# Optimization experiments

Hardware: AMD Instinct MI355X
Metric: run time of the kernel (lower is better)

Reference implementation:

```python
import jax, jax.numpy as jnp
import numpy as np

B, H, L, D = 2, 16, 2048, 64


def setup_inputs() -> dict:
    key = jax.random.key(0)
    kq, kk, kv = jax.random.split(key, 3)
    queries = jax.random.normal(kq, (B, H, L, D), dtype=jnp.float32)
    keys = jax.random.normal(kk, (B, H, L, D), dtype=jnp.float32)
    values = jax.random.normal(kv, (B, H, L, D), dtype=jnp.float32)
    # causal mask: True = masked (as consumed by masked_fill in the original)
    attn_mask = jnp.triu(jnp.ones((L, L), dtype=bool), k=1)
    return {"queries": queries, "keys": keys, "values": values, "attn_mask": attn_mask}


def reference(queries, keys, values, attn_mask):
    D_ = queries.shape[-1]
    scale = 1.0 / jnp.sqrt(jnp.asarray(D_, dtype=queries.dtype))
    # [B,H,Lq,Lk] score matrix (faithfully materialized as in the original)
    scores = jnp.einsum("bhqd,bhkd->bhqk", queries, keys) * scale
    scores = jnp.where(attn_mask, jnp.asarray(-1e9, dtype=scores.dtype), scores)
    attention = jax.nn.softmax(scores, axis=-1)
    # dropout rate = 0.0 (inference); identity
    out = jnp.einsum("bhqk,bhkd->bhqd", attention, values)
    return out
```

## Files before the change

kernel.cpp:

```cpp
#include <hip/hip_runtime.h>


constexpr int Lq = 2048;
constexpr int Dh = 64;
constexpr int QB = 64;
constexpr int KV = 64;
constexpr int RSTR = 144;
constexpr int IMG  = 64 * RSTR;
constexpr int TILEB = 2 * IMG;

typedef __attribute__((ext_vector_type(16))) float f32x16;
typedef __attribute__((ext_vector_type(4))) float f32x4;
typedef __attribute__((ext_vector_type(8))) unsigned short u16x8;
typedef __attribute__((ext_vector_type(4))) unsigned int u32x4;
typedef __attribute__((ext_vector_type(8))) __bf16 bf16x8;

__device__ __forceinline__ unsigned short f2bf(float f) {
  __bf16 h = (__bf16)f;
  return __builtin_bit_cast(unsigned short, h);
}
__device__ __forceinline__ unsigned pack2(float a, float b) {
  return (unsigned)f2bf(a) | ((unsigned)f2bf(b) << 16);
}
__device__ __forceinline__ f32x16 mfma32(u16x8 a, u16x8 b, f32x16 c) {
  return __builtin_amdgcn_mfma_f32_32x32x16_bf16(
      __builtin_bit_cast(bf16x8, a), __builtin_bit_cast(bf16x8, b), c, 0, 0, 0);
}
__device__ __forceinline__ void plswap(unsigned a, unsigned b,
                                       unsigned& wlo, unsigned& whi) {
#if __has_builtin(__builtin_amdgcn_permlane32_swap)
  auto r = __builtin_amdgcn_permlane32_swap((int)a, (int)b, false, false);
  wlo = (unsigned)r[0];
  whi = (unsigned)r[1];
#else
  const int hh = (threadIdx.x >> 5) & 1;
  unsigned pa = (unsigned)__shfl_xor((int)a, 32);
  unsigned pb = (unsigned)__shfl_xor((int)b, 32);
  wlo = hh ? pb : a;
  whi = hh ? b : pa;
#endif
}
__device__ __forceinline__ void glds16(const void* g, void* l) {
  __builtin_amdgcn_global_load_lds(
      (const __attribute__((address_space(1))) unsigned int*)g,
      (__attribute__((address_space(3))) unsigned int*)l, 16, 0, 0);
}

__global__ __launch_bounds__(256, 2)
void repack(const float* __restrict__ K, const float* __restrict__ V,
            unsigned char* __restrict__ W) {
  __shared__ unsigned short Vl[64][72];

  const int tid = threadIdx.x;
  const int bt  = blockIdx.x;
  const int bh  = bt >> 5;
  const int tl  = bt & 31;
  const size_t src = (size_t)bh * Lq * Dh + (size_t)tl * KV * Dh;
  unsigned char* img = W + (size_t)bt * TILEB;

  {
    const int kv = tid >> 2;
    const int c  = (tid & 3) * 2;
    const float* kp = K + src + (size_t)kv * Dh + c * 8;
    f32x4 a = *(const f32x4*)kp;
    f32x4 b = *(const f32x4*)(kp + 4);
    f32x4 cc = *(const f32x4*)(kp + 8);
    f32x4 d = *(const f32x4*)(kp + 12);
    u16x8 lo, hi;
    #pragma unroll
    for (int j = 0; j < 4; ++j) {
      lo[j] = f2bf(a[j]); lo[4 + j] = f2bf(b[j]);
      hi[j] = f2bf(cc[j]); hi[4 + j] = f2bf(d[j]);
    }
    *(u16x8*)(img + kv * RSTR + c * 16)      = lo;
    *(u16x8*)(img + kv * RSTR + c * 16 + 16) = hi;
  }
  {
    const int kv = tid >> 2;
    const int d0 = (tid & 3) * 16;
    const float* vp = V + src + (size_t)kv * Dh + d0;
    f32x4 a = *(const f32x4*)vp;
    f32x4 b = *(const f32x4*)(vp + 4);
    f32x4 cc = *(const f32x4*)(vp + 8);
    f32x4 d = *(const f32x4*)(vp + 12);
    u16x8 lo, hi;
    #pragma unroll
    for (int j = 0; j < 4; ++j) {
      lo[j] = f2bf(a[j]); lo[4 + j] = f2bf(b[j]);
      hi[j] = f2bf(cc[j]); hi[4 + j] = f2bf(d[j]);
    }
    *(u16x8*)&Vl[kv][d0]     = lo;
    *(u16x8*)&Vl[kv][d0 + 8] = hi;
  }
  __syncthreads();
  {
    const int d = tid >> 2;
    const int c = (tid & 3) * 2;
    u16x8 lo, hi;
    #pragma unroll
    for (int e = 0; e < 8; ++e) { lo[e] = Vl[c * 8 + e][d]; hi[e] = Vl[c * 8 + 8 + e][d]; }
    *(u16x8*)(img + IMG + d * RSTR + c * 16)       = lo;
    *(u16x8*)(img + IMG + d * RSTR + (c + 1) * 16) = hi;
  }
}

__global__ __launch_bounds__(256, 4)
void fattn_fwd(const float* __restrict__ Q, const unsigned char* __restrict__ W,
               float* __restrict__ O) {
  __shared__ __align__(16) unsigned char sm[2][TILEB];

  const int tid  = threadIdx.x;
  const int lane = tid & 63;
  const int w    = tid >> 6;
  const int l31  = lane & 31;
  const int h    = lane >> 5;
  const int qg   = w >> 1;
  const int kh   = w & 1;

  const int bid = blockIdx.x;
  const int xcd = bid & 7;
  const int s_  = bid >> 3;
  const int u   = s_ & 31;
  const int k   = s_ >> 5;
  const int bh  = xcd * 4 + k;
  const int qt  = (k & 1) ? u : (31 - u);
  const int qb  = qt * QB;
  const int n   = qt + 1;
  const size_t base = (size_t)bh * Lq * Dh;

  u16x8 qc[4];
  {
    const float* qp = Q + base + (size_t)(qb + qg * 32 + l31) * Dh + h * 8;
    #pragma unroll
    for (int dc = 0; dc < 4; ++dc) {
      f32x4 lo = *(const f32x4*)(qp + dc * 16);
      f32x4 hi = *(const f32x4*)(qp + dc * 16 + 4);
      u16x8 f;
      #pragma unroll
      for (int j = 0; j < 4; ++j) { f[j] = f2bf(lo[j]); f[4 + j] = f2bf(hi[j]); }
      qc[dc] = f;
    }
  }

  auto issue = [&](int t, int c) {
    const unsigned char* g = W + (size_t)(bh * 32 + t) * TILEB;
    unsigned char* dst = &sm[c][0];
    #pragma unroll
    for (int r = 0; r < 4; ++r)
      glds16(g + r * 4096 + w * 1024 + (lane << 4),
             dst + r * 4096 + w * 1024);
    if (w < 2)
      glds16(g + 16384 + w * 1024 + (lane << 4),
             dst + 16384 + w * 1024);
  };

  f32x16 accO0, accO1;
  #pragma unroll
  for (int i = 0; i < 16; ++i) { accO0[i] = 0.f; accO1[i] = 0.f; }
  float ls0 = 0.f, ls1 = 0.f, ls2 = 0.f, ls3 = 0.f;

  const float C1 = 0.125f * 1.4426950408889634f;
  const float C0 = -10.0f * 1.4426950408889634f;

  issue(0, 0);
  __syncthreads();

  for (int t = 0; t < n; ++t) {
    const int cur = t & 1;
    if (t + 1 < n) issue(t + 1, cur ^ 1);

    const unsigned char* smK = &sm[cur][0];
    const unsigned char* smV = &sm[cur][0] + IMG;
    const int kv0  = t * KV + kh * 32;
    const int qmin = qb + qg * 32;

    if (kv0 <= qmin + 31) {
      f32x16 s;
      #pragma unroll
      for (int i = 0; i < 16; ++i) s[i] = 0.f;
      __builtin_amdgcn_s_setprio(1);
      #pragma unroll
      for (int dc = 0; dc < 4; ++dc) {
        u16x8 kf = *(const u16x8*)(smK + (kh * 32 + l31) * RSTR + (dc * 2 + h) * 16);
        s = mfma32(kf, qc[dc], s);
      }
      __builtin_amdgcn_s_setprio(0);

      float p[16];
      if ((kv0 + 31) > qmin) {
        const int qrow = qmin + l31;
        #pragma unroll
        for (int r = 0; r < 16; ++r) {
          float e = __builtin_amdgcn_exp2f(s[r] * C1 + C0);
          const int kvg = kv0 + (r & 3) + 8 * (r >> 2) + 4 * h;
          p[r] = (kvg <= qrow) ? e : 0.0f;
        }
      } else {
        #pragma unroll
        for (int r = 0; r < 16; ++r)
          p[r] = __builtin_amdgcn_exp2f(s[r] * C1 + C0);
      }
      ls0 += (p[0] + p[1]) + (p[2] + p[3]);
      ls1 += (p[4] + p[5]) + (p[6] + p[7]);
      ls2 += (p[8] + p[9]) + (p[10] + p[11]);
      ls3 += (p[12] + p[13]) + (p[14] + p[15]);

      unsigned pk[4][2];
      #pragma unroll
      for (int q4 = 0; q4 < 4; ++q4) {
        pk[q4][0] = pack2(p[q4 * 4 + 0], p[q4 * 4 + 1]);
        pk[q4][1] = pack2(p[q4 * 4 + 2], p[q4 * 4 + 3]);
      }
      __builtin_amdgcn_s_setprio(1);
      #pragma unroll
      for (int c2 = 0; c2 < 2; ++c2) {
        unsigned w0, w1, w2, w3;
        plswap(pk[2 * c2][0], pk[2 * c2 + 1][0], w0, w2);
        plswap(pk[2 * c2][1], pk[2 * c2 + 1][1], w1, w3);
        u32x4 pw = {w0, w1, w2, w3};
        u16x8 pf = __builtin_bit_cast(u16x8, pw);
        const int vchunk = (kh * 4 + c2 * 2 + h) * 16;
        u16x8 vf0 = *(const u16x8*)(smV + l31 * RSTR + vchunk);
        u16x8 vf1 = *(const u16x8*)(smV + (32 + l31) * RSTR + vchunk);
        accO0 = mfma32(vf0, pf, accO0);
        accO1 = mfma32(vf1, pf, accO1);
      }
      __builtin_amdgcn_s_setprio(0);
    }
    __syncthreads();
  }

  const float lsum = (ls0 + ls1) + (ls2 + ls3);
  float* Mrg = (float*)&sm[0][0];
  if (kh == 1) {
    float* m = Mrg + (qg * 64 + lane) * 33;
    #pragma unroll
    for (int r = 0; r < 16; ++r) { m[r] = accO0[r]; m[16 + r] = accO1[r]; }
    m[32] = lsum;
  }
  __syncthreads();
  if (kh == 0) {
    const float* m = Mrg + (qg * 64 + lane) * 33;
    float ls = lsum + m[32];
    ls += __shfl_xor(ls, 32);
    const float inv = 1.0f / ls;
    float* op = O + base + (size_t)(qb + qg * 32 + l31) * Dh;
    #pragma unroll
    for (int r = 0; r < 16; ++r) {
      const int d = (r & 3) + 8 * (r >> 2) + 4 * h;
      op[d]      = (accO0[r] + m[r]) * inv;
      op[32 + d] = (accO1[r] + m[16 + r]) * inv;
    }
  }
}

extern "C" void kernel_launch(void* const* d_in, const int* in_sizes, int n_in,
                              void* d_out, int out_size, void* d_ws, size_t ws_size,
                              hipStream_t stream) {
  const float* Q = (const float*)d_in[0];
  const float* K = (const float*)d_in[1];
  const float* V = (const float*)d_in[2];
  float* O = (float*)d_out;
  unsigned char* W = (unsigned char*)d_ws;

  repack<<<dim3(1024), dim3(256), 0, stream>>>(K, V, W);
  fattn_fwd<<<dim3(1024), dim3(256), 0, stream>>>(Q, W, O);
}
```

Measured before the change: 50.82 us.

## Load K/V fragments directly from global into registers, dropping LDS staging

The repack step now writes K and V tiles in a fragment-major layout, so each lane's MFMA operand is one contiguous 16-byte chunk. The attention kernel then reads K and V fragments straight from global memory into registers with a software double buffer, instead of staging whole tiles in LDS with global_load_lds. Each wave also runs only its own causal tile count, which removes the per-tile block barriers. The cost is redundant global/L2 reads across waves, since the two q-group waves share K/V, and higher register pressure, so launch bounds drop to 3 blocks per CU.

```diff
diff --git a/kernel.cpp b/kernel.cpp
--- a/kernel.cpp
+++ b/kernel.cpp
@@ -5,9 +5,8 @@
 constexpr int Dh = 64;
 constexpr int QB = 64;
 constexpr int KV = 64;
-constexpr int RSTR = 144;
-constexpr int IMG  = 64 * RSTR;
-constexpr int TILEB = 2 * IMG;
+constexpr int TILEB = 16384;
+constexpr int VOFF  = 8192;
 
 typedef __attribute__((ext_vector_type(16))) float f32x16;
 typedef __attribute__((ext_vector_type(4))) float f32x4;
@@ -40,11 +39,6 @@
   whi = hh ? b : pa;
 #endif
 }
-__device__ __forceinline__ void glds16(const void* g, void* l) {
-  __builtin_amdgcn_global_load_lds(
-      (const __attribute__((address_space(1))) unsigned int*)g,
-      (__attribute__((address_space(3))) unsigned int*)l, 16, 0, 0);
-}
 
 __global__ __launch_bounds__(256, 2)
 void repack(const float* __restrict__ K, const float* __restrict__ V,
@@ -58,56 +52,56 @@
   const size_t src = (size_t)bh * Lq * Dh + (size_t)tl * KV * Dh;
   unsigned char* img = W + (size_t)bt * TILEB;
 
-  {
-    const int kv = tid >> 2;
-    const int c  = (tid & 3) * 2;
-    const float* kp = K + src + (size_t)kv * Dh + c * 8;
+  const int r  = tid >> 2;
+  const int c2 = (tid & 3) * 2;
+
+  {
+    const float* kp = K + src + (size_t)r * Dh + c2 * 8;
     f32x4 a = *(const f32x4*)kp;
     f32x4 b = *(const f32x4*)(kp + 4);
-    f32x4 cc = *(const f32x4*)(kp + 8);
+    f32x4 c = *(const f32x4*)(kp + 8);
     f32x4 d = *(const f32x4*)(kp + 12);
     u16x8 lo, hi;
     #pragma unroll
     for (int j = 0; j < 4; ++j) {
       lo[j] = f2bf(a[j]); lo[4 + j] = f2bf(b[j]);
-      hi[j] = f2bf(cc[j]); hi[4 + j] = f2bf(d[j]);
-    }
-    *(u16x8*)(img + kv * RSTR + c * 16)      = lo;
-    *(u16x8*)(img + kv * RSTR + c * 16 + 16) = hi;
-  }
-  {
-    const int kv = tid >> 2;
-    const int d0 = (tid & 3) * 16;
-    const float* vp = V + src + (size_t)kv * Dh + d0;
+      hi[j] = f2bf(c[j]); hi[4 + j] = f2bf(d[j]);
+    }
+    *(u16x8*)(img + (c2 * 64 + r) * 16)       = lo;
+    *(u16x8*)(img + ((c2 + 1) * 64 + r) * 16) = hi;
+  }
+  {
+    const float* vp = V + src + (size_t)r * Dh + c2 * 8;
     f32x4 a = *(const f32x4*)vp;
     f32x4 b = *(const f32x4*)(vp + 4);
-    f32x4 cc = *(const f32x4*)(vp + 8);
+    f32x4 c = *(const f32x4*)(vp + 8);
     f32x4 d = *(const f32x4*)(vp + 12);
     u16x8 lo, hi;
     #pragma unroll
     for (int j = 0; j < 4; ++j) {
       lo[j] = f2bf(a[j]); lo[4 + j] = f2bf(b[j]);
-      hi[j] = f2bf(cc[j]); hi[4 + j] = f2bf(d[j]);
-    }
-    *(u16x8*)&Vl[kv][d0]     = lo;
-    *(u16x8*)&Vl[kv][d0 + 8] = hi;
+      hi[j] = f2bf(c[j]); hi[4 + j] = f2bf(d[j]);
+    }
+    *(u16x8*)&Vl[r][c2 * 8]     = lo;
+    *(u16x8*)&Vl[r][c2 * 8 + 8] = hi;
   }
   __syncthreads();
   {
-    const int d = tid >> 2;
-    const int c = (tid & 3) * 2;
     u16x8 lo, hi;
     #pragma unroll
-    for (int e = 0; e < 8; ++e) { lo[e] = Vl[c * 8 + e][d]; hi[e] = Vl[c * 8 + 8 + e][d]; }
-    *(u16x8*)(img + IMG + d * RSTR + c * 16)       = lo;
-    *(u16x8*)(img + IMG + d * RSTR + (c + 1) * 16) = hi;
-  }
-}
-
-__global__ __launch_bounds__(256, 4)
+    for (int e = 0; e < 8; ++e) {
+      lo[e] = Vl[c2 * 8 + e][r];
+      hi[e] = Vl[c2 * 8 + 8 + e][r];
+    }
+    *(u16x8*)(img + VOFF + (c2 * 64 + r) * 16)       = lo;
+    *(u16x8*)(img + VOFF + ((c2 + 1) * 64 + r) * 16) = hi;
+  }
+}
+
+__global__ __launch_bounds__(256, 3)
 void fattn_fwd(const float* __restrict__ Q, const unsigned char* __restrict__ W,
                float* __restrict__ O) {
-  __shared__ __align__(16) unsigned char sm[2][TILEB];
+  __shared__ float Mrg[2][64][33];
 
   const int tid  = threadIdx.x;
   const int lane = tid & 63;
@@ -125,7 +119,6 @@
   const int bh  = xcd * 4 + k;
   const int qt  = (k & 1) ? u : (31 - u);
   const int qb  = qt * QB;
-  const int n   = qt + 1;
   const size_t base = (size_t)bh * Lq * Dh;
 
   u16x8 qc[4];
@@ -142,17 +135,11 @@
     }
   }
 
-  auto issue = [&](int t, int c) {
-    const unsigned char* g = W + (size_t)(bh * 32 + t) * TILEB;
-    unsigned char* dst = &sm[c][0];
-    #pragma unroll
-    for (int r = 0; r < 4; ++r)
-      glds16(g + r * 4096 + w * 1024 + (lane << 4),
-             dst + r * 4096 + w * 1024);
-    if (w < 2)
-      glds16(g + 16384 + w * 1024 + (lane << 4),
-             dst + 16384 + w * 1024);
-  };
+  const int qmin   = qb + qg * 32;
+  const int lastkv = qmin + 31 - kh * 32;
+  const int nw     = (lastkv >= 0) ? (lastkv >> 6) + 1 : 0;
+
+  const unsigned char* Wb = W + (size_t)(bh * 32) * TILEB;
 
   f32x16 accO0, accO1;
   #pragma unroll
@@ -162,85 +149,102 @@
   const float C1 = 0.125f * 1.4426950408889634f;
   const float C0 = -10.0f * 1.4426950408889634f;
 
-  issue(0, 0);
+  auto ldK = [&](u16x8 (&kf)[4], int t) {
+    const unsigned char* p = Wb + (size_t)t * TILEB + (kh * 32 + l31) * 16;
+    #pragma unroll
+    for (int dc = 0; dc < 4; ++dc)
+      kf[dc] = *(const u16x8*)(p + (dc * 2 + h) * 1024);
+  };
+  auto ldV = [&](u16x8 (&vf)[4], int t) {
+    const unsigned char* p =
+        Wb + (size_t)t * TILEB + VOFF + (kh * 4 + h) * 1024 + l31 * 16;
+    #pragma unroll
+    for (int c2 = 0; c2 < 2; ++c2) {
+      vf[c2 * 2 + 0] = *(const u16x8*)(p + c2 * 2048);
+      vf[c2 * 2 + 1] = *(const u16x8*)(p + c2 * 2048 + 512);
+    }
+  };
+
+  auto compute = [&](u16x8 (&kf)[4], u16x8 (&vf)[4], int t) {
+    const int kv0 = t * 64 + kh * 32;
+    f32x16 s;
+    #pragma unroll
+    for (int i = 0; i < 16; ++i) s[i] = 0.f;
+    __builtin_amdgcn_s_setprio(1);
+    #pragma unroll
+    for (int dc = 0; dc < 4; ++dc) s = mfma32(kf[dc], qc[dc], s);
+    __builtin_amdgcn_s_setprio(0);
+
+    float p[16];
+    if (kv0 + 31 > qmin) {
+      const int qrow = qmin + l31;
+      #pragma unroll
+      for (int r = 0; r < 16; ++r) {
+        float e = __builtin_amdgcn_exp2f(s[r] * C1 + C0);
+        const int kvg = kv0 + (r & 3) + 8 * (r >> 2) + 4 * h;
+        p[r] = (kvg <= qrow) ? e : 0.0f;
+      }
+    } else {
+      #pragma unroll
+      for (int r = 0; r < 16; ++r)
+        p[r] = __builtin_amdgcn_exp2f(s[r] * C1 + C0);
+    }
+    ls0 += (p[0] + p[1]) + (p[2] + p[3]);
+    ls1 += (p[4] + p[5]) + (p[6] + p[7]);
+    ls2 += (p[8] + p[9]) + (p[10] + p[11]);
+    ls3 += (p[12] + p[13]) + (p[14] + p[15]);
+
+    unsigned pk[4][2];
+    #pragma unroll
+    for (int q4 = 0; q4 < 4; ++q4) {
+      pk[q4][0] = pack2(p[q4 * 4 + 0], p[q4 * 4 + 1]);
+      pk[q4][1] = pack2(p[q4 * 4 + 2], p[q4 * 4 + 3]);
+    }
+    __builtin_amdgcn_s_setprio(1);
+    #pragma unroll
+    for (int c2 = 0; c2 < 2; ++c2) {
+      unsigned w0, w1, w2, w3;
+      plswap(pk[2 * c2][0], pk[2 * c2 + 1][0], w0, w2);
+      plswap(pk[2 * c2][1], pk[2 * c2 + 1][1], w1, w3);
+      u32x4 pw = {w0, w1, w2, w3};
+      u16x8 pf = __builtin_bit_cast(u16x8, pw);
+      accO0 = mfma32(vf[c2 * 2 + 0], pf, accO0);
+      accO1 = mfma32(vf[c2 * 2 + 1], pf, accO1);
+    }
+    __builtin_amdgcn_s_setprio(0);
+  };
+
+  if (nw > 0) {
+    u16x8 kA[4], kB[4], vv[4];
+    ldK(kA, 0);
+    int t = 0;
+    while (t + 2 <= nw) {
+      ldK(kB, t + 1);
+      ldV(vv, t);
+      compute(kA, vv, t);
+      const int tn = (t + 2 < nw) ? (t + 2) : (nw - 1);
+      ldK(kA, tn);
+      ldV(vv, t + 1);
+      compute(kB, vv, t + 1);
+      t += 2;
+    }
+    if (t < nw) {
+      ldV(vv, t);
+      compute(kA, vv, t);
+    }
+  }
+
+  const float lsum = (ls0 + ls1) + (ls2 + ls3);
   __syncthreads();
-
-  for (int t = 0; t < n; ++t) {
-    const int cur = t & 1;
-    if (t + 1 < n) issue(t + 1, cur ^ 1);
-
-    const unsigned char* smK = &sm[cur][0];
-    const unsigned char* smV = &sm[cur][0] + IMG;
-    const int kv0  = t * KV + kh * 32;
-    const int qmin = qb + qg * 32;
-
-    if (kv0 <= qmin + 31) {
-      f32x16 s;
-      #pragma unroll
-      for (int i = 0; i < 16; ++i) s[i] = 0.f;
-      __builtin_amdgcn_s_setprio(1);
-      #pragma unroll
-      for (int dc = 0; dc < 4; ++dc) {
-        u16x8 kf = *(const u16x8*)(smK + (kh * 32 + l31) * RSTR + (dc * 2 + h) * 16);
-        s = mfma32(kf, qc[dc], s);
-      }
-      __builtin_amdgcn_s_setprio(0);
-
-      float p[16];
-      if ((kv0 + 31) > qmin) {
-        const int qrow = qmin + l31;
-        #pragma unroll
-        for (int r = 0; r < 16; ++r) {
-          float e = __builtin_amdgcn_exp2f(s[r] * C1 + C0);
-          const int kvg = kv0 + (r & 3) + 8 * (r >> 2) + 4 * h;
-          p[r] = (kvg <= qrow) ? e : 0.0f;
-        }
-      } else {
-        #pragma unroll
-        for (int r = 0; r < 16; ++r)
-          p[r] = __builtin_amdgcn_exp2f(s[r] * C1 + C0);
-      }
-      ls0 += (p[0] + p[1]) + (p[2] + p[3]);
-      ls1 += (p[4] + p[5]) + (p[6] + p[7]);
-      ls2 += (p[8] + p[9]) + (p[10] + p[11]);
-      ls3 += (p[12] + p[13]) + (p[14] + p[15]);
-
-      unsigned pk[4][2];
-      #pragma unroll
-      for (int q4 = 0; q4 < 4; ++q4) {
-        pk[q4][0] = pack2(p[q4 * 4 + 0], p[q4 * 4 + 1]);
-        pk[q4][1] = pack2(p[q4 * 4 + 2], p[q4 * 4 + 3]);
-      }
-      __builtin_amdgcn_s_setprio(1);
-      #pragma unroll
-      for (int c2 = 0; c2 < 2; ++c2) {
-        unsigned w0, w1, w2, w3;
-        plswap(pk[2 * c2][0], pk[2 * c2 + 1][0], w0, w2);
-        plswap(pk[2 * c2][1], pk[2 * c2 + 1][1], w1, w3);
-        u32x4 pw = {w0, w1, w2, w3};
-        u16x8 pf = __builtin_bit_cast(u16x8, pw);
-        const int vchunk = (kh * 4 + c2 * 2 + h) * 16;
-        u16x8 vf0 = *(const u16x8*)(smV + l31 * RSTR + vchunk);
-        u16x8 vf1 = *(const u16x8*)(smV + (32 + l31) * RSTR + vchunk);
-        accO0 = mfma32(vf0, pf, accO0);
-        accO1 = mfma32(vf1, pf, accO1);
-      }
-      __builtin_amdgcn_s_setprio(0);
-    }
-    __syncthreads();
-  }
-
-  const float lsum = (ls0 + ls1) + (ls2 + ls3);
-  float* Mrg = (float*)&sm[0][0];
   if (kh == 1) {
-    float* m = Mrg + (qg * 64 + lane) * 33;
+    float* m = &Mrg[qg][lane][0];
     #pragma unroll
     for (int r = 0; r < 16; ++r) { m[r] = accO0[r]; m[16 + r] = accO1[r]; }
     m[32] = lsum;
   }
   __syncthreads();
   if (kh == 0) {
-    const float* m = Mrg + (qg * 64 + lane) * 33;
+    const float* m = &Mrg[qg][lane][0];
     float ls = lsum + m[32];
     ls += __shfl_xor(ls, 32);
     const float inv = 1.0f / ls;
```

New measurement: 52.18 us. 2.7% more time.
